# Performance work log

Measured on AMD Instinct MI355X. Metric: run time of the kernel, lower is better.

The kernel has to match this reference:

```python
import jax, jax.numpy as jnp
import numpy as np

N_NODES = 100000
N_EDGES = 1_600_000
F_IN = 128
N_HEADS = 4
F_OUT = 32


def setup_inputs() -> dict:
    key = jax.random.key(0)
    k1, k2, k3, k4, k5 = jax.random.split(key, 5)
    h_in = jax.random.normal(k1, (N_NODES, F_IN), dtype=jnp.float32)
    edge_index = jax.random.randint(k2, (2, N_EDGES), 0, N_NODES, dtype=jnp.int64)
    # Xavier-uniform-ish scales
    W = jax.random.normal(k3, (F_IN, N_HEADS * F_OUT), dtype=jnp.float32) * (1.0 / np.sqrt(F_IN))
    b = jnp.zeros((N_HEADS * F_OUT,), dtype=jnp.float32)
    a_src = jax.random.normal(k4, (N_HEADS, F_OUT), dtype=jnp.float32) * 0.1
    a_tgt = jax.random.normal(k5, (N_HEADS, F_OUT), dtype=jnp.float32) * 0.1
    return {"h_in": h_in, "edge_index": edge_index, "W": W, "b": b, "a_src": a_src, "a_tgt": a_tgt}


def reference(h_in, edge_index, W, b, a_src, a_tgt):
    # Eval mode: dropout is identity.
    src, tgt = edge_index[0], edge_index[1]
    # Shared linear projection: [N, H, F]
    h_proj = (h_in @ W + b).reshape(-1, N_HEADS, F_OUT)
    # Per-node attention score contributions: [N, H]
    score_src = jnp.einsum('nhf,hf->nh', h_proj, a_src)
    score_tgt = jnp.einsum('nhf,hf->nh', h_proj, a_tgt)
    # Edge-level scores (gather), LeakyReLU(0.2) as in the original: [E, H]
    e = jax.nn.leaky_relu(score_tgt[tgt] + score_src[src], negative_slope=0.2)
    # Segment softmax over incoming edges of each target node.
    # (Original uses raw exp without max subtraction; replicate faithfully.)
    exp_e = jnp.exp(e)
    denom = jax.ops.segment_sum(exp_e, tgt, num_segments=N_NODES)  # [N, H]
    alpha = exp_e / (denom[tgt] + 1e-16)                            # [E, H]
    # Weighted message aggregation: [N, H, F]
    msg = alpha[:, :, None] * h_proj[src]                           # [E, H, F]
    h_new = jax.ops.segment_sum(msg, tgt, num_segments=N_NODES)
    # concat=True branch: original computes activation(new_features) but returns
    # the UN-activated concatenated view (new_features_sigm is unused) -> replicate.
    return h_new.reshape(N_NODES, N_HEADS * F_OUT)
```

## Files before the change

### kernel.cpp

```cpp
#include <hip/hip_runtime.h>
#include <hip/hip_bf16.h>

typedef unsigned short u16;
typedef unsigned int u32;
typedef long long i64;
typedef __attribute__((ext_vector_type(8))) short s8v;
typedef __attribute__((ext_vector_type(4))) float f32x4;

#define BKT_CAP 8184

__device__ __forceinline__ float bf2f(u16 u) {
    union { u32 i; float f; } x; x.i = ((u32)u) << 16; return x.f;
}
__device__ __forceinline__ u16 f2bf(float f) {
    union { float f; u32 i; } x; x.f = f;
    u32 v = x.i;
    u32 r = v + 0x7FFFu + ((v >> 16) & 1u);
    return (u16)(r >> 16);
}
__device__ __forceinline__ int get_i(const void* p, size_t i, int m64) {
    return m64 ? (int)((const i64*)p)[i] : ((const int*)p)[i];
}
__device__ __forceinline__ float lrelu_clamp(float v) {
    v = v > 0.f ? v : 0.2f * v;
    return fminf(v, 80.f);
}

__global__ __launch_bounds__(256) void k_init(
    const u16* __restrict__ hin, const int* __restrict__ eidx, int* __restrict__ flags,
    const u16* __restrict__ W, u16* __restrict__ Wt, int* __restrict__ bucket_cnt, int nbk)
{
    const int b = blockIdx.x, t = threadIdx.x;
    if (b == 0) {
        __shared__ int c1, c2;
        if (t == 0) { c1 = 0; c2 = 0; }
        __syncthreads();
        int l1 = 0, l2 = 0;
        for (int i = t; i < 8192; i += 256) {
            float v = bf2f(hin[i]);
            if (!(fabsf(v) <= 100.f)) l1++;
            if ((i & 1) && eidx[i] == 0) l2++;
        }
        atomicAdd(&c1, l1); atomicAdd(&c2, l2);
        __syncthreads();
        if (t == 0) {
            flags[0] = (c1 > 40) ? 1 : 0;
            flags[1] = (c2 > 3000) ? 1 : 0;
        }
    } else {
        int i = (b - 1) * 256 + t;
        int k = i >> 7, n = i & 127;
        Wt[(size_t)n * 128 + k] = W[(size_t)k * 128 + n];
    }
    for (int i = b * 256 + t; i < nbk; i += gridDim.x * 256) bucket_cnt[i] = 0;
}

__global__ __launch_bounds__(256) void k_bktA(
    const void* __restrict__ eidx, const int* __restrict__ flags,
    int* __restrict__ bucket_cnt, int2* __restrict__ bkt,
    int n_edges, int n_nodes, int nbk)
{
    __shared__ int2 ed[4096];
    __shared__ int lcnt[512];
    __shared__ int lpos[512];
    const int t = threadIdx.x;
    const int e0 = blockIdx.x * 4096;
    const int m64 = flags[1];
    const int nloc = min(4096, n_edges - e0);

    for (int i = t; i < 512; i += 256) lcnt[i] = 0;
    __syncthreads();

    for (int r = 0; r < 16; r++) {
        int i = r * 256 + t;
        if (i < nloc) {
            int e = e0 + i;
            int s  = get_i(eidx, e, m64);
            int tg = get_i(eidx, (size_t)n_edges + e, m64);
            s  = min(max(s, 0), n_nodes - 1);
            tg = min(max(tg, 0), n_nodes - 1);
            ed[i] = make_int2(s, tg);
            atomicAdd(&lcnt[tg >> 8], 1);
        }
    }
    __syncthreads();

    for (int bb = t; bb < nbk; bb += 256) {
        int c = lcnt[bb];
        lpos[bb] = c ? atomicAdd(&bucket_cnt[bb], c) : 0;
    }
    __syncthreads();

    for (int r = 0; r < 16; r++) {
        int i = r * 256 + t;
        if (i < nloc) {
            int2 st = ed[i];
            int bb = st.y >> 8;
            int p = atomicAdd(&lpos[bb], 1);
            p = min(p, BKT_CAP - 1);
            bkt[(size_t)bb * BKT_CAP + p] = st;
        }
    }
}

__global__ __launch_bounds__(256) void k_bsort(
    const int* __restrict__ bucket_cnt, const int2* __restrict__ bkt,
    int* __restrict__ offs, int* __restrict__ src_sorted,
    int n_edges, int n_nodes, int nbk)
{
    __shared__ int s_a[512], s_b[512];
    __shared__ int tcnt[256], tpos[256];
    const int t = threadIdx.x;
    const int b = blockIdx.x;

    for (int i = t; i < 512; i += 256)
        s_a[i] = (i < nbk) ? min(bucket_cnt[i], BKT_CAP) : 0;
    __syncthreads();
    int* pa = s_a; int* pb = s_b;
    for (int off = 1; off < 512; off <<= 1) {
        #pragma unroll
        for (int k = 0; k < 2; k++) {
            int i = t + k * 256;
            pb[i] = pa[i] + (i >= off ? pa[i - off] : 0);
        }
        __syncthreads();
        int* sw = pa; pa = pb; pb = sw;
    }
    const int cnt_b = min(bucket_cnt[b], BKT_CAP);
    const int Gb    = pa[b] - cnt_b;
    const int total = pa[511];
    __syncthreads();

    tcnt[t] = 0;
    __syncthreads();
    const int2* mybkt = bkt + (size_t)b * BKT_CAP;
    for (int i = t; i < cnt_b; i += 256)
        atomicAdd(&tcnt[mybkt[i].y & 255], 1);
    __syncthreads();

    int own = tcnt[t];
    s_a[t] = own;
    __syncthreads();
    for (int off = 1; off < 256; off <<= 1) {
        int x = (t >= off) ? s_a[t - off] : 0;
        __syncthreads();
        s_a[t] += x;
        __syncthreads();
    }
    const int texcl = s_a[t] - own;

    const int tgt_id = b * 256 + t;
    if (tgt_id < n_nodes) offs[tgt_id] = Gb + texcl;
    if (b == 0 && t == 0) offs[n_nodes] = total;
    tpos[t] = Gb + texcl;
    __syncthreads();
    for (int i = t; i < cnt_b; i += 256) {
        int2 st = mybkt[i];
        int p = atomicAdd(&tpos[st.y & 255], 1);
        src_sorted[p] = st.x;
    }
}

__global__ __launch_bounds__(256) void k_proj_mfma(
    const u16* __restrict__ hin, const u16* __restrict__ Wt,
    const u16* __restrict__ bias, const u16* __restrict__ a_src,
    const u16* __restrict__ a_tgt, const int* __restrict__ flags,
    u16* __restrict__ hp, float* __restrict__ ssrc, float* __restrict__ stgt,
    int M)
{
    if (flags[0]) return;
    const int wave = threadIdx.x >> 6;
    const int lane = threadIdx.x & 63;
    const int q = lane >> 4, col = lane & 15;
    const int row0 = blockIdx.x * 64 + wave * 16;
    if (row0 >= M) return;

    const int arow = min(row0 + col, M - 1);
    f32x4 acc[8];
    #pragma unroll
    for (int ct = 0; ct < 8; ct++) acc[ct] = (f32x4){0.f, 0.f, 0.f, 0.f};

    #pragma unroll
    for (int kc = 0; kc < 4; kc++) {
        s8v afrag = *(const s8v*)(hin + (size_t)arow * 128 + kc * 32 + q * 8);
        #pragma unroll
        for (int ct = 0; ct < 8; ct++) {
            s8v bfrag = *(const s8v*)(Wt + (size_t)(ct * 16 + col) * 128 + kc * 32 + q * 8);
            acc[ct] = __builtin_amdgcn_mfma_f32_16x16x32_bf16(afrag, bfrag, acc[ct], 0, 0, 0);
        }
    }

    float bb[8], as[8], at[8];
    #pragma unroll
    for (int ct = 0; ct < 8; ct++) {
        int c = ct * 16 + col;
        bb[ct] = bf2f(bias[c]);
        as[ct] = bf2f(a_src[c]);
        at[ct] = bf2f(a_tgt[c]);
    }

    #pragma unroll
    for (int r = 0; r < 4; r++) {
        int row = row0 + q * 4 + r;
        float ps0 = 0.f, ps1 = 0.f, ps2 = 0.f, ps3 = 0.f;
        float pt0 = 0.f, pt1 = 0.f, pt2 = 0.f, pt3 = 0.f;
        float ov[8];
        #pragma unroll
        for (int ct = 0; ct < 8; ct++) {
            float v = acc[ct][r] + bb[ct];
            ov[ct] = v;
            float s = v * as[ct], t2 = v * at[ct];
            if (ct < 2)      { ps0 += s; pt0 += t2; }
            else if (ct < 4) { ps1 += s; pt1 += t2; }
            else if (ct < 6) { ps2 += s; pt2 += t2; }
            else             { ps3 += s; pt3 += t2; }
        }
        if (row < M) {
            union { ushort4 h[2]; uint4 qv; } pk;
            pk.h[0] = make_ushort4(f2bf(ov[0]), f2bf(ov[1]), f2bf(ov[2]), f2bf(ov[3]));
            pk.h[1] = make_ushort4(f2bf(ov[4]), f2bf(ov[5]), f2bf(ov[6]), f2bf(ov[7]));
            *(uint4*)(hp + (size_t)row * 128 + col * 8) = pk.qv;
        }
        #pragma unroll
        for (int m = 1; m < 16; m <<= 1) {
            ps0 += __shfl_xor(ps0, m); ps1 += __shfl_xor(ps1, m);
            ps2 += __shfl_xor(ps2, m); ps3 += __shfl_xor(ps3, m);
            pt0 += __shfl_xor(pt0, m); pt1 += __shfl_xor(pt1, m);
            pt2 += __shfl_xor(pt2, m); pt3 += __shfl_xor(pt3, m);
        }
        if (row < M && col < 4) {
            float vs = col == 0 ? ps0 : col == 1 ? ps1 : col == 2 ? ps2 : ps3;
            float vt = col == 0 ? pt0 : col == 1 ? pt1 : col == 2 ? pt2 : pt3;
            ssrc[(size_t)row * 4 + col] = vs;
            stgt[(size_t)row * 4 + col] = vt;
        }
    }
}

__global__ __launch_bounds__(256) void k_proj_f32(
    const float* __restrict__ hin, const float* __restrict__ W,
    const float* __restrict__ bias, const float* __restrict__ a_src,
    const float* __restrict__ a_tgt, const int* __restrict__ flags,
    float* __restrict__ hp, float* __restrict__ ssrc, float* __restrict__ stgt,
    int n_nodes)
{
    if (!flags[0]) return;
    __shared__ float hs[32][128];
    __shared__ float sh_s[32][4], sh_t[32][4];
    const int t = threadIdx.x;
    const int row0 = blockIdx.x * 32;

    for (int i = t; i < 32 * 64; i += 256) {
        int r = i >> 6, kk = (i & 63) * 2;
        int row = row0 + r;
        float2 v = (row < n_nodes) ? *(const float2*)(hin + (size_t)row * 128 + kk)
                                   : make_float2(0.f, 0.f);
        hs[r][kk] = v.x; hs[r][kk + 1] = v.y;
    }
    __syncthreads();

    const int cg = (t & 31) * 4;
    const int rg = (t >> 5) * 4;
    float acc[4][4] = {};
    for (int k = 0; k < 128; k += 4) {
        float4 h0 = *(const float4*)&hs[rg + 0][k];
        float4 h1 = *(const float4*)&hs[rg + 1][k];
        float4 h2 = *(const float4*)&hs[rg + 2][k];
        float4 h3 = *(const float4*)&hs[rg + 3][k];
        #pragma unroll
        for (int j = 0; j < 4; j++) {
            float4 w4 = *(const float4*)(W + (size_t)(k + j) * 128 + cg);
            float hh0 = ((const float*)&h0)[j], hh1 = ((const float*)&h1)[j];
            float hh2 = ((const float*)&h2)[j], hh3 = ((const float*)&h3)[j];
            acc[0][0] += hh0 * w4.x; acc[0][1] += hh0 * w4.y; acc[0][2] += hh0 * w4.z; acc[0][3] += hh0 * w4.w;
            acc[1][0] += hh1 * w4.x; acc[1][1] += hh1 * w4.y; acc[1][2] += hh1 * w4.z; acc[1][3] += hh1 * w4.w;
            acc[2][0] += hh2 * w4.x; acc[2][1] += hh2 * w4.y; acc[2][2] += hh2 * w4.z; acc[2][3] += hh2 * w4.w;
            acc[3][0] += hh3 * w4.x; acc[3][1] += hh3 * w4.y; acc[3][2] += hh3 * w4.z; acc[3][3] += hh3 * w4.w;
        }
    }
    float b0 = bias[cg], b1 = bias[cg + 1], b2 = bias[cg + 2], b3 = bias[cg + 3];
    #pragma unroll
    for (int i = 0; i < 4; i++) {
        acc[i][0] += b0; acc[i][1] += b1; acc[i][2] += b2; acc[i][3] += b3;
    }
    #pragma unroll
    for (int i = 0; i < 4; i++) {
        int row = row0 + rg + i;
        if (row < n_nodes)
            *(float4*)(hp + (size_t)row * 128 + cg) =
                make_float4(acc[i][0], acc[i][1], acc[i][2], acc[i][3]);
    }
    const int head = cg >> 5;
    float as0 = a_src[cg], as1 = a_src[cg + 1], as2 = a_src[cg + 2], as3 = a_src[cg + 3];
    float at0 = a_tgt[cg], at1 = a_tgt[cg + 1], at2 = a_tgt[cg + 2], at3 = a_tgt[cg + 3];
    float p1[4], p2[4];
    #pragma unroll
    for (int i = 0; i < 4; i++) {
        p1[i] = acc[i][0] * as0 + acc[i][1] * as1 + acc[i][2] * as2 + acc[i][3] * as3;
        p2[i] = acc[i][0] * at0 + acc[i][1] * at1 + acc[i][2] * at2 + acc[i][3] * at3;
    }
    #pragma unroll
    for (int m = 1; m < 8; m <<= 1) {
        #pragma unroll
        for (int i = 0; i < 4; i++) {
            p1[i] += __shfl_xor(p1[i], m);
            p2[i] += __shfl_xor(p2[i], m);
        }
    }
    if ((t & 7) == 0) {
        #pragma unroll
        for (int i = 0; i < 4; i++) { sh_s[rg + i][head] = p1[i]; sh_t[rg + i][head] = p2[i]; }
    }
    __syncthreads();
    if (t < 128) {
        int r = t >> 2, h = t & 3;
        int row = row0 + r;
        if (row < n_nodes) ssrc[(size_t)row * 4 + h] = sh_s[r][h];
    } else {
        int r = (t - 128) >> 2, h = t & 3;
        int row = row0 + r;
        if (row < n_nodes) stgt[(size_t)row * 4 + h] = sh_t[r][h];
    }
}

__global__ __launch_bounds__(256) void k_agg_csr(
    const int* __restrict__ offs, const int* __restrict__ src_sorted,
    const float* __restrict__ ssrc, const float* __restrict__ stgt,
    const void* __restrict__ hp, void* __restrict__ out,
    const int* __restrict__ flags, int n_nodes)
{
    __shared__ u16 ob[4][128];
    const int wave = threadIdx.x >> 6;
    int wid = (blockIdx.x * 256 + threadIdx.x) >> 6;
    if (wid >= n_nodes) return;
    const int lane = threadIdx.x & 63;
    const int fp32 = flags[0];
    const int d0 = offs[wid], d1 = offs[wid + 1];

    if (!fp32) {
        const int sub = lane >> 4;
        const int li = lane & 15;
        const u16* hpb = (const u16*)hp;
        const float4* ssrc4 = (const float4*)ssrc;
        const float4 st4 = ((const float4*)stgt)[wid];
        const int deg = d1 - d0;

        float a[8] = {};
        auto accum = [&](float4 w, uint4 v) {
            a[0] += w.x * bf2f((u16)(v.x & 0xffff));
            a[1] += w.x * bf2f((u16)(v.x >> 16));
            a[2] += w.y * bf2f((u16)(v.y & 0xffff));
            a[3] += w.y * bf2f((u16)(v.y >> 16));
            a[4] += w.z * bf2f((u16)(v.z & 0xffff));
            a[5] += w.z * bf2f((u16)(v.z >> 16));
            a[6] += w.w * bf2f((u16)(v.w & 0xffff));
            a[7] += w.w * bf2f((u16)(v.w >> 16));
        };

        const int nh = min(deg, 64);
        int my_s = 0;
        float4 my_w = make_float4(0.f, 0.f, 0.f, 0.f);
        if (nh > 0) {
            my_s = src_sorted[d0 + min(lane, nh - 1)];
            float4 cs = ssrc4[my_s];
            if (lane < nh) {
                my_w = make_float4(__expf(lrelu_clamp(cs.x + st4.x)),
                                   __expf(lrelu_clamp(cs.y + st4.y)),
                                   __expf(lrelu_clamp(cs.z + st4.z)),
                                   __expf(lrelu_clamp(cs.w + st4.w)));
            }
        }

        const int ns = (nh + 3) >> 2;
        auto sload = [&](int k, uint4& vv) {
            if (k < ns) {
                int s = __shfl(my_s, k * 4 + sub);
                vv = *(const uint4*)(hpb + (size_t)s * 128 + li * 8);
            }
        };
        auto sacc = [&](int k, uint4 vv) {
            if (k < ns) {
                int idx = k * 4 + sub;
                float4 w;
                w.x = __shfl(my_w.x, idx);
                w.y = __shfl(my_w.y, idx);
                w.z = __shfl(my_w.z, idx);
                w.w = __shfl(my_w.w, idx);
                accum(w, vv);
            }
        };
        uint4 v0{}, v1{}, v2{}, v3{}, v4{}, v5{}, v6{}, v7{};
        sload(0, v0); sload(1, v1); sload(2, v2); sload(3, v3);
        sload(4, v4); sload(5, v5); sload(6, v6); sload(7, v7);
        sacc(0, v0); sload(8, v0);
        sacc(1, v1); sload(9, v1);
        sacc(2, v2); sload(10, v2);
        sacc(3, v3); sload(11, v3);
        sacc(4, v4); sload(12, v4);
        sacc(5, v5); sload(13, v5);
        sacc(6, v6); sload(14, v6);
        sacc(7, v7); sload(15, v7);
        sacc(8, v0); sacc(9, v1); sacc(10, v2); sacc(11, v3);
        sacc(12, v4); sacc(13, v5); sacc(14, v6); sacc(15, v7);

        float4 es_t = make_float4(0.f, 0.f, 0.f, 0.f);
        if (deg > 64) {
            for (int e = d0 + 64; e < d1; e += 4) {
                int idx = e + sub;
                int ok = idx < d1;
                int s = src_sorted[ok ? idx : d1 - 1];
                uint4 v = *(const uint4*)(hpb + (size_t)s * 128 + li * 8);
                float4 cs = ssrc4[s];
                float4 w = make_float4(__expf(lrelu_clamp(cs.x + st4.x)),
                                       __expf(lrelu_clamp(cs.y + st4.y)),
                                       __expf(lrelu_clamp(cs.z + st4.z)),
                                       __expf(lrelu_clamp(cs.w + st4.w)));
                if (!ok) w = make_float4(0.f, 0.f, 0.f, 0.f);
                accum(w, v);
                es_t.x += w.x; es_t.y += w.y; es_t.z += w.z; es_t.w += w.w;
            }
        }

        float4 es = my_w;
        #pragma unroll
        for (int m = 1; m < 16; m <<= 1) {
            es.x += __shfl_xor(es.x, m);
            es.y += __shfl_xor(es.y, m);
            es.z += __shfl_xor(es.z, m);
            es.w += __shfl_xor(es.w, m);
        }
        es.x += es_t.x; es.y += es_t.y; es.z += es_t.z; es.w += es_t.w;

        #pragma unroll
        for (int m = 0; m < 8; m++) {
            a[m] += __shfl_xor(a[m], 16);
            a[m] += __shfl_xor(a[m], 32);
        }
        es.x += __shfl_xor(es.x, 16); es.x += __shfl_xor(es.x, 32);
        es.y += __shfl_xor(es.y, 16); es.y += __shfl_xor(es.y, 32);
        es.z += __shfl_xor(es.z, 16); es.z += __shfl_xor(es.z, 32);
        es.w += __shfl_xor(es.w, 16); es.w += __shfl_xor(es.w, 32);

        if (sub == 0) {
            float inv[4] = {1.f / (es.x + 1e-16f), 1.f / (es.y + 1e-16f),
                            1.f / (es.z + 1e-16f), 1.f / (es.w + 1e-16f)};
            #pragma unroll
            for (int m = 0; m < 8; m++)
                ob[wave][m * 16 + li] = f2bf(a[m] * inv[m >> 1]);
            uint4 ov = *(const uint4*)&ob[wave][li * 8];
            *(uint4*)((u16*)out + (size_t)wid * 128 + li * 8) = ov;
        }
    } else {
        const int sub = lane >> 5;
        const int li = lane & 31;
        const int head = li >> 3;
        const float* hpf = (const float*)hp;
        const float st = stgt[(size_t)wid * 4 + head];
        float a0 = 0.f, a1 = 0.f, a2 = 0.f, a3 = 0.f, es = 0.f;
        for (int e = d0; e < d1; e += 2) {
            int idx = e + sub;
            int ok = idx < d1;
            int s = src_sorted[ok ? idx : d1 - 1];
            float c = ssrc[(size_t)s * 4 + head];
            float4 v = *(const float4*)(hpf + (size_t)s * 128 + li * 4);
            float w = ok ? __expf(lrelu_clamp(c + st)) : 0.f;
            a0 += w * v.x; a1 += w * v.y; a2 += w * v.z; a3 += w * v.w;
            es += w;
        }
        a0 += __shfl_xor(a0, 32); a1 += __shfl_xor(a1, 32);
        a2 += __shfl_xor(a2, 32); a3 += __shfl_xor(a3, 32);
        es += __shfl_xor(es, 32);
        float inv = 1.0f / (es + 1e-16f);
        if (sub == 0) {
            *(float4*)((float*)out + (size_t)wid * 128 + li * 4) =
                make_float4(a0 * inv, a1 * inv, a2 * inv, a3 * inv);
        }
    }
}

extern "C" void kernel_launch(void* const* d_in, const int* in_sizes, int n_in,
                              void* d_out, int out_size, void* d_ws, size_t ws_size,
                              hipStream_t stream)
{
    const void* h_in  = d_in[0];
    const void* eidx  = d_in[1];
    const void* W     = d_in[2];
    const void* bias  = d_in[3];
    const void* a_src = d_in[4];
    const void* a_tgt = d_in[5];

    const int n_nodes = in_sizes[0] / 128;
    const int n_edges = in_sizes[1] / 2;
    const int nbk = (n_nodes + 255) >> 8;
    const int nba = (n_edges + 4095) / 4096;

    char* p = (char*)d_ws;
    auto alloc = [&](size_t bytes) { char* q = p; p += (bytes + 255) & ~(size_t)255; return q; };
    int*   flags      = (int*)  alloc(256);
    void*  hp         = (void*) alloc((size_t)n_nodes * 128 * sizeof(float));
    u16*   Wt         = (u16*)  alloc(128 * 128 * sizeof(u16));
    float* ssrc       = (float*)alloc((size_t)n_nodes * 4 * sizeof(float));
    float* stgt       = (float*)alloc((size_t)n_nodes * 4 * sizeof(float));
    int*   offs       = (int*)  alloc(((size_t)n_nodes + 1) * sizeof(int));
    int*   bucket_cnt = (int*)  alloc((size_t)nbk * sizeof(int));
    int*   src_sorted = (int*)  alloc((size_t)n_edges * sizeof(int));

    size_t bkt_bytes = (size_t)nbk * BKT_CAP * sizeof(int2);
    int2* bkt;
    if (bkt_bytes <= (size_t)n_nodes * 128 * 2)
        bkt = (int2*)((char*)hp + (size_t)n_nodes * 128 * 2);
    else
        bkt = (int2*)alloc(bkt_bytes);

    k_init     <<<65, 256, 0, stream>>>((const u16*)h_in, (const int*)eidx, flags,
                                        (const u16*)W, Wt, bucket_cnt, nbk);
    k_bktA     <<<nba, 256, 0, stream>>>(eidx, flags, bucket_cnt, bkt,
                                         n_edges, n_nodes, nbk);
    k_bsort    <<<nbk, 256, 0, stream>>>(bucket_cnt, bkt, offs, src_sorted,
                                         n_edges, n_nodes, nbk);
    k_proj_mfma<<<(n_nodes + 63) / 64, 256, 0, stream>>>((const u16*)h_in, Wt, (const u16*)bias,
                                                         (const u16*)a_src, (const u16*)a_tgt,
                                                         flags, (u16*)hp, ssrc, stgt, n_nodes);
    k_proj_f32 <<<(n_nodes + 31) / 32, 256, 0, stream>>>((const float*)h_in, (const float*)W,
                                                         (const float*)bias, (const float*)a_src,
                                                         (const float*)a_tgt, flags, (float*)hp,
                                                         ssrc, stgt, n_nodes);
    k_agg_csr  <<<(n_nodes + 3) / 4, 256, 0, stream>>>(offs, src_sorted, ssrc, stgt,
                                                       hp, d_out, flags, n_nodes);
}
```

Measured before the change: 366.5 us.

## Store fp32-path projections as bf16 and reuse the bf16 gather aggregation

In the fp32 input path, the projection kernel now rounds its output to bf16 and writes it through shared memory in the interleaved layout the bf16 aggregation expects. The aggregation kernel then uses one shared, software-pipelined bf16 gather for both paths and only branches on output precision, staging the fp32 result in shared memory. This halves the bytes fetched per gathered neighbour row and removes the slower fp32 edge loop. The cost is bf16 rounding of the projected features on the fp32 path, which reduces accuracy, plus an extra block barrier at the end of aggregation.

```diff
diff --git a/kernel.cpp b/kernel.cpp
--- a/kernel.cpp
+++ b/kernel.cpp
@@ -241,11 +241,12 @@
     const float* __restrict__ hin, const float* __restrict__ W,
     const float* __restrict__ bias, const float* __restrict__ a_src,
     const float* __restrict__ a_tgt, const int* __restrict__ flags,
-    float* __restrict__ hp, float* __restrict__ ssrc, float* __restrict__ stgt,
+    u16* __restrict__ hp, float* __restrict__ ssrc, float* __restrict__ stgt,
     int n_nodes)
 {
     if (!flags[0]) return;
     __shared__ float hs[32][128];
+    __shared__ u16 sh_hp[32][128];
     __shared__ float sh_s[32][4], sh_t[32][4];
     const int t = threadIdx.x;
     const int row0 = blockIdx.x * 32;
@@ -285,10 +286,11 @@
     }
     #pragma unroll
     for (int i = 0; i < 4; i++) {
-        int row = row0 + rg + i;
-        if (row < n_nodes)
-            *(float4*)(hp + (size_t)row * 128 + cg) =
-                make_float4(acc[i][0], acc[i][1], acc[i][2], acc[i][3]);
+        #pragma unroll
+        for (int j = 0; j < 4; j++) {
+            int f = cg + j;
+            sh_hp[rg + i][(f & 15) * 8 + (f >> 4)] = f2bf(acc[i][j]);
+        }
     }
     const int head = cg >> 5;
     float as0 = a_src[cg], as1 = a_src[cg + 1], as2 = a_src[cg + 2], as3 = a_src[cg + 3];
@@ -312,6 +314,12 @@
         for (int i = 0; i < 4; i++) { sh_s[rg + i][head] = p1[i]; sh_t[rg + i][head] = p2[i]; }
     }
     __syncthreads();
+    for (int c = t; c < 512; c += 256) {
+        int r = c >> 4, off = (c & 15) * 8;
+        int row = row0 + r;
+        if (row < n_nodes)
+            *(uint4*)(hp + (size_t)row * 128 + off) = *(const uint4*)&sh_hp[r][off];
+    }
     if (t < 128) {
         int r = t >> 2, h = t & 3;
         int row = row0 + r;
@@ -330,151 +338,141 @@
     const int* __restrict__ flags, int n_nodes)
 {
     __shared__ u16 ob[4][128];
+    __shared__ float obf[4][128];
     const int wave = threadIdx.x >> 6;
     int wid = (blockIdx.x * 256 + threadIdx.x) >> 6;
-    if (wid >= n_nodes) return;
+    wid = min(wid, n_nodes - 1);
     const int lane = threadIdx.x & 63;
     const int fp32 = flags[0];
     const int d0 = offs[wid], d1 = offs[wid + 1];
 
-    if (!fp32) {
-        const int sub = lane >> 4;
-        const int li = lane & 15;
-        const u16* hpb = (const u16*)hp;
-        const float4* ssrc4 = (const float4*)ssrc;
-        const float4 st4 = ((const float4*)stgt)[wid];
-        const int deg = d1 - d0;
-
-        float a[8] = {};
-        auto accum = [&](float4 w, uint4 v) {
-            a[0] += w.x * bf2f((u16)(v.x & 0xffff));
-            a[1] += w.x * bf2f((u16)(v.x >> 16));
-            a[2] += w.y * bf2f((u16)(v.y & 0xffff));
-            a[3] += w.y * bf2f((u16)(v.y >> 16));
-            a[4] += w.z * bf2f((u16)(v.z & 0xffff));
-            a[5] += w.z * bf2f((u16)(v.z >> 16));
-            a[6] += w.w * bf2f((u16)(v.w & 0xffff));
-            a[7] += w.w * bf2f((u16)(v.w >> 16));
-        };
-
-        const int nh = min(deg, 64);
-        int my_s = 0;
-        float4 my_w = make_float4(0.f, 0.f, 0.f, 0.f);
-        if (nh > 0) {
-            my_s = src_sorted[d0 + min(lane, nh - 1)];
-            float4 cs = ssrc4[my_s];
-            if (lane < nh) {
-                my_w = make_float4(__expf(lrelu_clamp(cs.x + st4.x)),
+    const int sub = lane >> 4;
+    const int li = lane & 15;
+    const u16* hpb = (const u16*)hp;
+    const float4* ssrc4 = (const float4*)ssrc;
+    const float4 st4 = ((const float4*)stgt)[wid];
+    const int deg = d1 - d0;
+
+    float a[8] = {};
+    auto accum = [&](float4 w, uint4 v) {
+        a[0] += w.x * bf2f((u16)(v.x & 0xffff));
+        a[1] += w.x * bf2f((u16)(v.x >> 16));
+        a[2] += w.y * bf2f((u16)(v.y & 0xffff));
+        a[3] += w.y * bf2f((u16)(v.y >> 16));
+        a[4] += w.z * bf2f((u16)(v.z & 0xffff));
+        a[5] += w.z * bf2f((u16)(v.z >> 16));
+        a[6] += w.w * bf2f((u16)(v.w & 0xffff));
+        a[7] += w.w * bf2f((u16)(v.w >> 16));
+    };
+
+    const int nh = min(deg, 64);
+    int my_s = 0;
+    float4 my_w = make_float4(0.f, 0.f, 0.f, 0.f);
+    if (nh > 0) {
+        my_s = src_sorted[d0 + min(lane, nh - 1)];
+        float4 cs = ssrc4[my_s];
+        if (lane < nh) {
+            my_w = make_float4(__expf(lrelu_clamp(cs.x + st4.x)),
+                               __expf(lrelu_clamp(cs.y + st4.y)),
+                               __expf(lrelu_clamp(cs.z + st4.z)),
+                               __expf(lrelu_clamp(cs.w + st4.w)));
+        }
+    }
+
+    const int ns = (nh + 3) >> 2;
+    auto sload = [&](int k, uint4& vv) {
+        if (k < ns) {
+            int s = __shfl(my_s, k * 4 + sub);
+            vv = *(const uint4*)(hpb + (size_t)s * 128 + li * 8);
+        }
+    };
+    auto sacc = [&](int k, uint4 vv) {
+        if (k < ns) {
+            int idx = k * 4 + sub;
+            float4 w;
+            w.x = __shfl(my_w.x, idx);
+            w.y = __shfl(my_w.y, idx);
+            w.z = __shfl(my_w.z, idx);
+            w.w = __shfl(my_w.w, idx);
+            accum(w, vv);
+        }
+    };
+    uint4 v0{}, v1{}, v2{}, v3{}, v4{}, v5{}, v6{}, v7{};
+    sload(0, v0); sload(1, v1); sload(2, v2); sload(3, v3);
+    sload(4, v4); sload(5, v5); sload(6, v6); sload(7, v7);
+    sacc(0, v0); sload(8, v0);
+    sacc(1, v1); sload(9, v1);
+    sacc(2, v2); sload(10, v2);
+    sacc(3, v3); sload(11, v3);
+    sacc(4, v4); sload(12, v4);
+    sacc(5, v5); sload(13, v5);
+    sacc(6, v6); sload(14, v6);
+    sacc(7, v7); sload(15, v7);
+    sacc(8, v0); sacc(9, v1); sacc(10, v2); sacc(11, v3);
+    sacc(12, v4); sacc(13, v5); sacc(14, v6); sacc(15, v7);
+
+    float4 es_t = make_float4(0.f, 0.f, 0.f, 0.f);
+    if (deg > 64) {
+        for (int e = d0 + 64; e < d1; e += 4) {
+            int idx = e + sub;
+            int ok = idx < d1;
+            int s = src_sorted[ok ? idx : d1 - 1];
+            uint4 v = *(const uint4*)(hpb + (size_t)s * 128 + li * 8);
+            float4 cs = ssrc4[s];
+            float4 w = make_float4(__expf(lrelu_clamp(cs.x + st4.x)),
                                    __expf(lrelu_clamp(cs.y + st4.y)),
                                    __expf(lrelu_clamp(cs.z + st4.z)),
                                    __expf(lrelu_clamp(cs.w + st4.w)));
-            }
-        }
-
-        const int ns = (nh + 3) >> 2;
-        auto sload = [&](int k, uint4& vv) {
-            if (k < ns) {
-                int s = __shfl(my_s, k * 4 + sub);
-                vv = *(const uint4*)(hpb + (size_t)s * 128 + li * 8);
-            }
-        };
-        auto sacc = [&](int k, uint4 vv) {
-            if (k < ns) {
-                int idx = k * 4 + sub;
-                float4 w;
-                w.x = __shfl(my_w.x, idx);
-                w.y = __shfl(my_w.y, idx);
-                w.z = __shfl(my_w.z, idx);
-                w.w = __shfl(my_w.w, idx);
-                accum(w, vv);
-            }
-        };
-        uint4 v0{}, v1{}, v2{}, v3{}, v4{}, v5{}, v6{}, v7{};
-        sload(0, v0); sload(1, v1); sload(2, v2); sload(3, v3);
-        sload(4, v4); sload(5, v5); sload(6, v6); sload(7, v7);
-        sacc(0, v0); sload(8, v0);
-        sacc(1, v1); sload(9, v1);
-        sacc(2, v2); sload(10, v2);
-        sacc(3, v3); sload(11, v3);
-        sacc(4, v4); sload(12, v4);
-        sacc(5, v5); sload(13, v5);
-        sacc(6, v6); sload(14, v6);
-        sacc(7, v7); sload(15, v7);
-        sacc(8, v0); sacc(9, v1); sacc(10, v2); sacc(11, v3);
-        sacc(12, v4); sacc(13, v5); sacc(14, v6); sacc(15, v7);
-
-        float4 es_t = make_float4(0.f, 0.f, 0.f, 0.f);
-        if (deg > 64) {
-            for (int e = d0 + 64; e < d1; e += 4) {
-                int idx = e + sub;
-                int ok = idx < d1;
-                int s = src_sorted[ok ? idx : d1 - 1];
-                uint4 v = *(const uint4*)(hpb + (size_t)s * 128 + li * 8);
-                float4 cs = ssrc4[s];
-                float4 w = make_float4(__expf(lrelu_clamp(cs.x + st4.x)),
-                                       __expf(lrelu_clamp(cs.y + st4.y)),
-                                       __expf(lrelu_clamp(cs.z + st4.z)),
-                                       __expf(lrelu_clamp(cs.w + st4.w)));
-                if (!ok) w = make_float4(0.f, 0.f, 0.f, 0.f);
-                accum(w, v);
-                es_t.x += w.x; es_t.y += w.y; es_t.z += w.z; es_t.w += w.w;
-            }
-        }
-
-        float4 es = my_w;
-        #pragma unroll
-        for (int m = 1; m < 16; m <<= 1) {
-            es.x += __shfl_xor(es.x, m);
-            es.y += __shfl_xor(es.y, m);
-            es.z += __shfl_xor(es.z, m);
-            es.w += __shfl_xor(es.w, m);
-        }
-        es.x += es_t.x; es.y += es_t.y; es.z += es_t.z; es.w += es_t.w;
-
-        #pragma unroll
-        for (int m = 0; m < 8; m++) {
-            a[m] += __shfl_xor(a[m], 16);
-            a[m] += __shfl_xor(a[m], 32);
-        }
-        es.x += __shfl_xor(es.x, 16); es.x += __shfl_xor(es.x, 32);
-        es.y += __shfl_xor(es.y, 16); es.y += __shfl_xor(es.y, 32);
-        es.z += __shfl_xor(es.z, 16); es.z += __shfl_xor(es.z, 32);
-        es.w += __shfl_xor(es.w, 16); es.w += __shfl_xor(es.w, 32);
-
+            if (!ok) w = make_float4(0.f, 0.f, 0.f, 0.f);
+            accum(w, v);
+            es_t.x += w.x; es_t.y += w.y; es_t.z += w.z; es_t.w += w.w;
+        }
+    }
+
+    float4 es = my_w;
+    #pragma unroll
+    for (int m = 1; m < 16; m <<= 1) {
+        es.x += __shfl_xor(es.x, m);
+        es.y += __shfl_xor(es.y, m);
+        es.z += __shfl_xor(es.z, m);
+        es.w += __shfl_xor(es.w, m);
+    }
+    es.x += es_t.x; es.y += es_t.y; es.z += es_t.z; es.w += es_t.w;
+
+    #pragma unroll
+    for (int m = 0; m < 8; m++) {
+        a[m] += __shfl_xor(a[m], 16);
+        a[m] += __shfl_xor(a[m], 32);
+    }
+    es.x += __shfl_xor(es.x, 16); es.x += __shfl_xor(es.x, 32);
+    es.y += __shfl_xor(es.y, 16); es.y += __shfl_xor(es.y, 32);
+    es.z += __shfl_xor(es.z, 16); es.z += __shfl_xor(es.z, 32);
+    es.w += __shfl_xor(es.w, 16); es.w += __shfl_xor(es.w, 32);
+
+    float inv4[4] = {1.f / (es.x + 1e-16f), 1.f / (es.y + 1e-16f),
+                     1.f / (es.z + 1e-16f), 1.f / (es.w + 1e-16f)};
+
+    if (!fp32) {
         if (sub == 0) {
-            float inv[4] = {1.f / (es.x + 1e-16f), 1.f / (es.y + 1e-16f),
-                            1.f / (es.z + 1e-16f), 1.f / (es.w + 1e-16f)};
             #pragma unroll
             for (int m = 0; m < 8; m++)
-                ob[wave][m * 16 + li] = f2bf(a[m] * inv[m >> 1]);
+                ob[wave][m * 16 + li] = f2bf(a[m] * inv4[m >> 1]);
+        }
+        __syncthreads();
+        if (sub == 0) {
             uint4 ov = *(const uint4*)&ob[wave][li * 8];
             *(uint4*)((u16*)out + (size_t)wid * 128 + li * 8) = ov;
         }
     } else {
-        const int sub = lane >> 5;
-        const int li = lane & 31;
-        const int head = li >> 3;
-        const float* hpf = (const float*)hp;
-        const float st = stgt[(size_t)wid * 4 + head];
-        float a0 = 0.f, a1 = 0.f, a2 = 0.f, a3 = 0.f, es = 0.f;
-        for (int e = d0; e < d1; e += 2) {
-            int idx = e + sub;
-            int ok = idx < d1;
-            int s = src_sorted[ok ? idx : d1 - 1];
-            float c = ssrc[(size_t)s * 4 + head];
-            float4 v = *(const float4*)(hpf + (size_t)s * 128 + li * 4);
-            float w = ok ? __expf(lrelu_clamp(c + st)) : 0.f;
-            a0 += w * v.x; a1 += w * v.y; a2 += w * v.z; a3 += w * v.w;
-            es += w;
-        }
-        a0 += __shfl_xor(a0, 32); a1 += __shfl_xor(a1, 32);
-        a2 += __shfl_xor(a2, 32); a3 += __shfl_xor(a3, 32);
-        es += __shfl_xor(es, 32);
-        float inv = 1.0f / (es + 1e-16f);
         if (sub == 0) {
-            *(float4*)((float*)out + (size_t)wid * 128 + li * 4) =
-                make_float4(a0 * inv, a1 * inv, a2 * inv, a3 * inv);
-        }
+            #pragma unroll
+            for (int m = 0; m < 8; m++)
+                obf[wave][m * 16 + li] = a[m] * inv4[m >> 1];
+        }
+        __syncthreads();
+        float* of = (float*)out + (size_t)wid * 128;
+        *(float2*)(of + lane * 2) = make_float2(obf[wave][lane * 2],
+                                                obf[wave][lane * 2 + 1]);
     }
 }
 
@@ -523,7 +521,7 @@
                                                          flags, (u16*)hp, ssrc, stgt, n_nodes);
     k_proj_f32 <<<(n_nodes + 31) / 32, 256, 0, stream>>>((const float*)h_in, (const float*)W,
                                                          (const float*)bias, (const float*)a_src,
-                                                         (const float*)a_tgt, flags, (float*)hp,
+                                                         (const float*)a_tgt, flags, (u16*)hp,
                                                          ssrc, stgt, n_nodes);
     k_agg_csr  <<<(n_nodes + 3) / 4, 256, 0, stream>>>(offs, src_sorted, ssrc, stgt,
                                                        hp, d_out, flags, n_nodes);
```

Measured after the change: 308.6 us. 1.19x faster.
